# Optimization experiments

Hardware: AMD Instinct MI355X
Metric: run time of the kernel (lower is better)

The kernel has to match this reference:

```python
import jax, jax.numpy as jnp
import numpy as np

BATCH, T, D_MODEL, DIM = 8, 4096, 512, 512
R_MIN, R_MAX, MAX_PHASE = 0.0, 1.0, 6.28


def setup_inputs() -> dict:
    key = jax.random.key(0)
    ks = jax.random.split(key, 8)
    x = jax.random.normal(ks[0], (BATCH, T, D_MODEL), dtype=jnp.float32)
    h0 = jnp.zeros((BATCH, 1, DIM), dtype=jnp.float32)
    # nu_log / theta_log per the module's initializers
    u1 = jax.random.uniform(ks[1], (DIM,))
    nu_log = jnp.log(-0.5 * jnp.log(u1 * (R_MAX ** 2 - R_MIN ** 2) + R_MIN ** 2)).astype(jnp.float32)
    u2 = jax.random.uniform(ks[2], (DIM,))
    theta_log = jnp.log(MAX_PHASE * u2).astype(jnp.float32)
    # B ~ N(0,1)/sqrt(2*D_in), C ~ N(0,1)/sqrt(D_out)
    B_re = (jax.random.normal(ks[3], (D_MODEL, DIM)) / jnp.sqrt(2.0 * D_MODEL)).astype(jnp.float32)
    B_im = (jax.random.normal(ks[4], (D_MODEL, DIM)) / jnp.sqrt(2.0 * D_MODEL)).astype(jnp.float32)
    C_re = (jax.random.normal(ks[5], (DIM, D_MODEL)) / jnp.sqrt(float(D_MODEL))).astype(jnp.float32)
    C_im = (jax.random.normal(ks[6], (DIM, D_MODEL)) / jnp.sqrt(float(D_MODEL))).astype(jnp.float32)
    D_param = jax.random.normal(ks[7], (D_MODEL,)).astype(jnp.float32)
    # gamma_log = log(sqrt(1 - |Lambda|^2)) with Lambda from nu/theta
    diag_lambda = jnp.exp(-jnp.exp(nu_log) + 1j * jnp.exp(theta_log))
    gamma_log = jnp.log(jnp.sqrt(1.0 - jnp.abs(diag_lambda) ** 2)).astype(jnp.float32)
    return {"x": x, "h0": h0, "nu_log": nu_log, "theta_log": theta_log,
            "B_re": B_re, "B_im": B_im, "C_re": C_re, "C_im": C_im,
            "D_param": D_param, "gamma_log": gamma_log}


def _binary_op(ei, ej):
    a_i, b_i = ei
    a_j, b_j = ej
    return (a_j * a_i, a_j * b_i + b_j)


def reference(x, h0, nu_log, theta_log, B_re, B_im, C_re, C_im, D_param, gamma_log):
    B, T_len, _ = x.shape
    Lambda = jnp.exp(-jnp.exp(nu_log) + 1j * jnp.exp(theta_log))            # (N,) complex
    B_norm = (B_re + 1j * B_im) * jnp.exp(gamma_log)[None, :]               # (D,N) complex
    C = C_re + 1j * C_im                                                     # (N,D) complex
    # Input projection: Bu[b,t,n] = sum_d x[b,t,d] * B_norm[d,n]
    Bu = jnp.einsum('btd,dn->btn', x.astype(jnp.complex64), B_norm)
    Bu = jnp.concatenate([h0.astype(jnp.complex64), Bu], axis=1)             # (B,T+1,N)
    Lam = jnp.broadcast_to(Lambda, Bu.shape)                                 # (B,T+1,N)
    _, H = jax.lax.associative_scan(_binary_op, (Lam, Bu), axis=1)
    H = H[:, 1:]                                                             # (B,T,N)
    y = jnp.einsum('btn,nd->btd', H, C).real + D_param * x                   # (B,T,D)
    new_h = H[:, -1:]                                                        # (B,1,N) complex
    return (y, new_h)
```

## Files before the change

kernel.cpp:

```cpp
#include <hip/hip_runtime.h>

#define T_LEN 4096
#define DMODEL 512
#define DIM 512
#define NBATCH 8
#define MROWS (NBATCH * T_LEN)
#define NCHUNK 128
#define LCHUNK 32

typedef __attribute__((ext_vector_type(8))) short short8;
typedef __attribute__((ext_vector_type(4))) float float4v;

__device__ __forceinline__ ushort f2b(float f) {
    union { float fl; unsigned u; } v; v.fl = f;
    unsigned u = v.u;
    return (ushort)((u + 0x7FFFu + ((u >> 16) & 1u)) >> 16);
}
__device__ __forceinline__ float b2f(ushort u) {
    union { unsigned u; float f; } v; v.u = (unsigned)u << 16; return v.f;
}

__device__ __forceinline__ void glds16(const ushort* g, ushort* l) {
    __builtin_amdgcn_global_load_lds(
        (const __attribute__((address_space(1))) void*)g,
        (__attribute__((address_space(3))) void*)l, 16, 0, 0);
}


__global__ __launch_bounds__(256) void k_prep_x(const float* __restrict__ x,
                                                ushort* __restrict__ xb) {
    int i = (blockIdx.x * 256 + threadIdx.x) * 4;
    float4 v = *(const float4*)(x + i);
    ushort4 o;
    o.x = f2b(v.x); o.y = f2b(v.y); o.z = f2b(v.z); o.w = f2b(v.w);
    *(ushort4*)(xb + i) = o;
}

__global__ __launch_bounds__(256) void k_prep_B(const float* __restrict__ Bre,
                                                const float* __restrict__ Bim,
                                                const float* __restrict__ gamma_log,
                                                ushort* __restrict__ BT) {
    int idx = blockIdx.x * 256 + threadIdx.x;
    int n = idx >> 9;
    int d = idx & 511;
    float v;
    if (n < 512) v = Bre[d * 512 + n] * __expf(gamma_log[n]);
    else { int nn = n - 512; v = Bim[d * 512 + nn] * __expf(gamma_log[nn]); }
    BT[idx] = f2b(v);
}

__global__ __launch_bounds__(256) void k_prep_C(const float* __restrict__ Cre,
                                                const float* __restrict__ Cim,
                                                ushort* __restrict__ CT) {
    int idx = blockIdx.x * 256 + threadIdx.x;
    int d = idx >> 10;
    int k = idx & 1023;
    float v = (k < 512) ? Cre[k * 512 + d] : -Cim[(k - 512) * 512 + d];
    CT[idx] = f2b(v);
}

template<int K, int MODE, int NBN>
__global__ __launch_bounds__(256) void k_gemm(
    const ushort* __restrict__ A, const ushort* __restrict__ Bt,
    ushort* __restrict__ oRe, ushort* __restrict__ oIm,
    float* __restrict__ y, const float* __restrict__ x, const float* __restrict__ Dp) {
    __shared__ ushort sA[128 * 64];
    __shared__ ushort sB[128 * 64];
    const int tid = threadIdx.x;
    const int L = blockIdx.x;
    const int xcd = L & 7;
    const int slot = L >> 3;
    const int m0 = (xcd * 32 + slot / NBN) * 128;
    const int n0 = (slot % NBN) * 128;
    const int wave = tid >> 6;
    const int lane = tid & 63;
    const int wm = (wave >> 1) * 64;
    const int wn = (wave & 1) * 64;
    const int lr = lane & 15;
    const int quad = lane >> 4;

    const int srow = lane >> 3;
    const int schunk = (lane & 7) ^ srow;
    const ushort* gA0 = A + (size_t)(m0 + wave * 32 + srow) * K + schunk * 8;
    const ushort* gB0 = Bt + (size_t)(n0 + wave * 32 + srow) * K + schunk * 8;

    float4v acc[4][4];
#pragma unroll
    for (int i = 0; i < 4; i++)
#pragma unroll
        for (int j = 0; j < 4; j++) {
            float4v z = {0.f, 0.f, 0.f, 0.f};
            acc[i][j] = z;
        }

    for (int k0 = 0; k0 < K; k0 += 64) {
        __syncthreads();
#pragma unroll
        for (int c = 0; c < 4; c++) {
            glds16(gA0 + (size_t)(c * 8) * K + k0, &sA[(wave * 32 + c * 8) * 64]);
            glds16(gB0 + (size_t)(c * 8) * K + k0, &sB[(wave * 32 + c * 8) * 64]);
        }
        __syncthreads();

#pragma unroll
        for (int kk = 0; kk < 2; kk++) {
            short8 af[4], bfr[4];
#pragma unroll
            for (int i = 0; i < 4; i++) {
                int row = wm + i * 16 + lr;
                af[i] = *(const short8*)&sA[row * 64 + (((kk * 4 + quad) ^ (row & 7)) * 8)];
            }
#pragma unroll
            for (int j = 0; j < 4; j++) {
                int row = wn + j * 16 + lr;
                bfr[j] = *(const short8*)&sB[row * 64 + (((kk * 4 + quad) ^ (row & 7)) * 8)];
            }
#pragma unroll
            for (int i = 0; i < 4; i++)
#pragma unroll
                for (int j = 0; j < 4; j++)
                    acc[i][j] = __builtin_amdgcn_mfma_f32_16x16x32_bf16(af[i], bfr[j], acc[i][j], 0, 0, 0);
        }
    }

#pragma unroll
    for (int i = 0; i < 4; i++) {
#pragma unroll
        for (int j = 0; j < 4; j++) {
            int gmb = m0 + wm + i * 16 + quad * 4;
            int gn = n0 + wn + j * 16 + lr;
#pragma unroll
            for (int r = 0; r < 4; r++) {
                float v = acc[i][j][r];
                int row = gmb + r;
                if (MODE == 1) {
                    if (gn < 512) oRe[(size_t)row * 512 + gn] = f2b(v);
                    else oIm[(size_t)row * 512 + (gn - 512)] = f2b(v);
                } else {
                    size_t o = (size_t)row * 512 + gn;
                    y[o] = v + Dp[gn] * x[o];
                }
            }
        }
    }
}


__device__ __forceinline__ void lambda_of(const float* nu_log, const float* theta_log,
                                          int n, float& lre, float& lim) {
    float e = __expf(nu_log[n]);
    float th = __expf(theta_log[n]);
    float rad = __expf(-e);
    float s, c;
    __sincosf(th, &s, &c);
    lre = rad * c;
    lim = rad * s;
}

__global__ __launch_bounds__(256) void k_scan1(const ushort* __restrict__ BuRe,
                                               const ushort* __restrict__ BuIm,
                                               const float* __restrict__ nu_log,
                                               const float* __restrict__ theta_log,
                                               float* __restrict__ cRe, float* __restrict__ cIm) {
    int n2 = threadIdx.x;
    int b = blockIdx.x >> 7;
    int c = blockIdx.x & 127;
    float lre0, lim0, lre1, lim1;
    lambda_of(nu_log, theta_log, 2 * n2, lre0, lim0);
    lambda_of(nu_log, theta_log, 2 * n2 + 1, lre1, lim1);
    float hr0 = 0.f, hi0 = 0.f, hr1 = 0.f, hi1 = 0.f;
    size_t base = ((size_t)b * T_LEN + (size_t)c * LCHUNK) * 512 + 2 * n2;
#pragma unroll 8
    for (int j = 0; j < LCHUNK; j++) {
        ushort2 ur = *(const ushort2*)(BuRe + base + (size_t)j * 512);
        ushort2 ui = *(const ushort2*)(BuIm + base + (size_t)j * 512);
        float br0 = b2f(ur.x), br1 = b2f(ur.y), bi0 = b2f(ui.x), bi1 = b2f(ui.y);
        float nr0 = lre0 * hr0 - lim0 * hi0 + br0;
        float ni0 = lre0 * hi0 + lim0 * hr0 + bi0;
        hr0 = nr0; hi0 = ni0;
        float nr1 = lre1 * hr1 - lim1 * hi1 + br1;
        float ni1 = lre1 * hi1 + lim1 * hr1 + bi1;
        hr1 = nr1; hi1 = ni1;
    }
    size_t co = ((size_t)b * NCHUNK + c) * 512 + 2 * n2;
    *(float2*)(cRe + co) = make_float2(hr0, hr1);
    *(float2*)(cIm + co) = make_float2(hi0, hi1);
}

__global__ __launch_bounds__(64) void k_scan2(const float* __restrict__ cRe,
                                              const float* __restrict__ cIm,
                                              const float* __restrict__ h0,
                                              const float* __restrict__ nu_log,
                                              const float* __restrict__ theta_log,
                                              float* __restrict__ pRe, float* __restrict__ pIm,
                                              float* __restrict__ newH, int newh_mode) {
    int idx = blockIdx.x * 64 + threadIdx.x;
    int b = idx >> 9;
    int n = idx & 511;
    float lre, lim;
    lambda_of(nu_log, theta_log, n, lre, lim);
    float Lr = lre, Li = lim;
#pragma unroll
    for (int s = 0; s < 5; s++) {
        float nr = Lr * Lr - Li * Li;
        float ni = 2.f * Lr * Li;
        Lr = nr; Li = ni;
    }
    float cr = h0[b * 512 + n];
    float ci = 0.f;
#pragma unroll 4
    for (int c = 0; c < NCHUNK; c++) {
        size_t o = ((size_t)b * NCHUNK + c) * 512 + n;
        pRe[o] = cr;
        pIm[o] = ci;
        float ar = cRe[o], ai = cIm[o];
        float nr = Lr * cr - Li * ci + ar;
        float ni = Lr * ci + Li * cr + ai;
        cr = nr; ci = ni;
    }
    size_t ci_idx = (size_t)b * 512 + n;
    if (newh_mode == 1) {
        newH[ci_idx] = cr;
        newH[(size_t)NBATCH * 512 + ci_idx] = ci;
    } else if (newh_mode == 2) {
        newH[ci_idx] = cr;
    } else {
        newH[ci_idx * 2] = cr;
        newH[ci_idx * 2 + 1] = ci;
    }
}

__global__ __launch_bounds__(256) void k_scan3(const ushort* __restrict__ BuRe,
                                               const ushort* __restrict__ BuIm,
                                               const float* __restrict__ pRe,
                                               const float* __restrict__ pIm,
                                               const float* __restrict__ nu_log,
                                               const float* __restrict__ theta_log,
                                               ushort* __restrict__ Hbf) {
    int n2 = threadIdx.x;
    int b = blockIdx.x >> 7;
    int c = blockIdx.x & 127;
    float lre0, lim0, lre1, lim1;
    lambda_of(nu_log, theta_log, 2 * n2, lre0, lim0);
    lambda_of(nu_log, theta_log, 2 * n2 + 1, lre1, lim1);
    size_t co = ((size_t)b * NCHUNK + c) * 512 + 2 * n2;
    float2 frv = *(const float2*)(pRe + co);
    float2 fiv = *(const float2*)(pIm + co);
    float fr0 = frv.x, fr1 = frv.y, fi0 = fiv.x, fi1 = fiv.y;
    float pr0 = lre0, pi0 = lim0, pr1 = lre1, pi1 = lim1;
    float hr0 = 0.f, hi0 = 0.f, hr1 = 0.f, hi1 = 0.f;
    size_t row0 = (size_t)b * T_LEN + (size_t)c * LCHUNK;
#pragma unroll 4
    for (int j = 0; j < LCHUNK; j++) {
        size_t base = (row0 + j) * 512 + 2 * n2;
        ushort2 ur = *(const ushort2*)(BuRe + base);
        ushort2 ui = *(const ushort2*)(BuIm + base);
        float br0 = b2f(ur.x), br1 = b2f(ur.y), bi0 = b2f(ui.x), bi1 = b2f(ui.y);
        float nr0 = lre0 * hr0 - lim0 * hi0 + br0;
        float ni0 = lre0 * hi0 + lim0 * hr0 + bi0;
        hr0 = nr0; hi0 = ni0;
        float nr1 = lre1 * hr1 - lim1 * hi1 + br1;
        float ni1 = lre1 * hi1 + lim1 * hr1 + bi1;
        hr1 = nr1; hi1 = ni1;
        float vr0 = hr0 + pr0 * fr0 - pi0 * fi0;
        float vi0 = hi0 + pr0 * fi0 + pi0 * fr0;
        float vr1 = hr1 + pr1 * fr1 - pi1 * fi1;
        float vi1 = hi1 + pr1 * fi1 + pi1 * fr1;
        size_t hrow = (row0 + j) * 1024;
        ushort2 wre, wim;
        wre.x = f2b(vr0); wre.y = f2b(vr1);
        wim.x = f2b(vi0); wim.y = f2b(vi1);
        *(ushort2*)(Hbf + hrow + 2 * n2) = wre;
        *(ushort2*)(Hbf + hrow + 512 + 2 * n2) = wim;
        float npr0 = pr0 * lre0 - pi0 * lim0;
        float npi0 = pr0 * lim0 + pi0 * lre0;
        pr0 = npr0; pi0 = npi0;
        float npr1 = pr1 * lre1 - pi1 * lim1;
        float npi1 = pr1 * lim1 + pi1 * lre1;
        pr1 = npr1; pi1 = npi1;
    }
}


extern "C" void kernel_launch(void* const* d_in, const int* in_sizes, int n_in,
                              void* d_out, int out_size, void* d_ws, size_t ws_size,
                              hipStream_t stream) {
    const float* x         = (const float*)d_in[0];
    const float* h0        = (const float*)d_in[1];
    const float* nu_log    = (const float*)d_in[2];
    const float* theta_log = (const float*)d_in[3];
    const float* B_re      = (const float*)d_in[4];
    const float* B_im      = (const float*)d_in[5];
    const float* C_re      = (const float*)d_in[6];
    const float* C_im      = (const float*)d_in[7];
    const float* D_param   = (const float*)d_in[8];
    const float* gamma_log = (const float*)d_in[9];

    char* ws = (char*)d_ws;
    size_t off = 0;
    ushort* Xb   = (ushort*)(ws + off); off += (size_t)MROWS * 512 * 2;
    ushort* BT   = (ushort*)(ws + off); off += (size_t)1024 * 512 * 2;
    ushort* CT   = (ushort*)(ws + off); off += (size_t)512 * 1024 * 2;
    ushort* BuRe = (ushort*)(ws + off); off += (size_t)MROWS * 512 * 2;
    ushort* BuIm = (ushort*)(ws + off); off += (size_t)MROWS * 512 * 2;
    ushort* Hbf  = (ushort*)(ws + off); off += (size_t)MROWS * 1024 * 2;
    float*  cRe  = (float*)(ws + off); off += (size_t)NBATCH * NCHUNK * 512 * 4;
    float*  cIm  = (float*)(ws + off); off += (size_t)NBATCH * NCHUNK * 512 * 4;
    float*  pRe  = (float*)(ws + off); off += (size_t)NBATCH * NCHUNK * 512 * 4;
    float*  pIm  = (float*)(ws + off); off += (size_t)NBATCH * NCHUNK * 512 * 4;

    float* y_out = (float*)d_out;
    float* newH  = (float*)d_out + (size_t)MROWS * 512;

    const int tail = out_size - MROWS * 512;
    int newh_mode = 0;
    if (tail == NBATCH * 512 * 2) newh_mode = 1;
    else if (tail == NBATCH * 512) newh_mode = 2;

    k_prep_x<<<dim3(MROWS * 512 / 4 / 256), dim3(256), 0, stream>>>(x, Xb);
    k_prep_B<<<dim3(1024 * 512 / 256), dim3(256), 0, stream>>>(B_re, B_im, gamma_log, BT);
    k_prep_C<<<dim3(512 * 1024 / 256), dim3(256), 0, stream>>>(C_re, C_im, CT);

    k_gemm<512, 1, 8><<<dim3(2048), dim3(256), 0, stream>>>(
        Xb, BT, BuRe, BuIm, nullptr, nullptr, nullptr);

    k_scan1<<<dim3(NBATCH * NCHUNK), dim3(256), 0, stream>>>(BuRe, BuIm, nu_log, theta_log, cRe, cIm);
    k_scan2<<<dim3(NBATCH * 512 / 64), dim3(64), 0, stream>>>(cRe, cIm, h0, nu_log, theta_log, pRe, pIm, newH, newh_mode);
    k_scan3<<<dim3(NBATCH * NCHUNK), dim3(256), 0, stream>>>(BuRe, BuIm, pRe, pIm, nu_log, theta_log, Hbf);

    k_gemm<1024, 2, 4><<<dim3(1024), dim3(256), 0, stream>>>(
        Hbf, CT, nullptr, nullptr, y_out, x, D_param);
}
```

Baseline: 292.5 us.

## Store Bu channel-major, vectorize scan loads, merge prep kernels, halve chunk count

The first GEMM now writes Bu transposed (channel-major, time contiguous) as 4-wide bf16 stores. This lets scan1 and scan3 read 8 consecutive timesteps per channel with 16-byte loads instead of strided 4-byte loads. The chunk split changes from 128x32 to 64x64, and the chunk-power exponent in scan2 is adjusted to match. The three prep kernels are merged into one launch. The risks are per-thread strided access across channels in the scan (each thread touches different rows) and fewer blocks in the scan kernels.

New measurement: 421.5 us. 44.1% more time.

```diff
diff --git a/kernel.cpp b/kernel.cpp
--- a/kernel.cpp
+++ b/kernel.cpp
@@ -5,8 +5,8 @@
 #define DIM 512
 #define NBATCH 8
 #define MROWS (NBATCH * T_LEN)
-#define NCHUNK 128
-#define LCHUNK 32
+#define NCHUNK 64
+#define LCHUNK 64
 
 typedef __attribute__((ext_vector_type(8))) short short8;
 typedef __attribute__((ext_vector_type(4))) float float4v;
@@ -19,6 +19,12 @@
 __device__ __forceinline__ float b2f(ushort u) {
     union { unsigned u; float f; } v; v.u = (unsigned)u << 16; return v.f;
 }
+__device__ __forceinline__ float bflo(unsigned u) {
+    union { unsigned x; float f; } v; v.x = u << 16; return v.f;
+}
+__device__ __forceinline__ float bfhi(unsigned u) {
+    union { unsigned x; float f; } v; v.x = u & 0xffff0000u; return v.f;
+}
 
 __device__ __forceinline__ void glds16(const ushort* g, ushort* l) {
     __builtin_amdgcn_global_load_lds(
@@ -26,37 +32,38 @@
         (__attribute__((address_space(3))) void*)l, 16, 0, 0);
 }
 
-
-__global__ __launch_bounds__(256) void k_prep_x(const float* __restrict__ x,
-                                                ushort* __restrict__ xb) {
-    int i = (blockIdx.x * 256 + threadIdx.x) * 4;
-    float4 v = *(const float4*)(x + i);
-    ushort4 o;
-    o.x = f2b(v.x); o.y = f2b(v.y); o.z = f2b(v.z); o.w = f2b(v.w);
-    *(ushort4*)(xb + i) = o;
-}
-
-__global__ __launch_bounds__(256) void k_prep_B(const float* __restrict__ Bre,
-                                                const float* __restrict__ Bim,
-                                                const float* __restrict__ gamma_log,
-                                                ushort* __restrict__ BT) {
-    int idx = blockIdx.x * 256 + threadIdx.x;
-    int n = idx >> 9;
-    int d = idx & 511;
-    float v;
-    if (n < 512) v = Bre[d * 512 + n] * __expf(gamma_log[n]);
-    else { int nn = n - 512; v = Bim[d * 512 + nn] * __expf(gamma_log[nn]); }
-    BT[idx] = f2b(v);
-}
-
-__global__ __launch_bounds__(256) void k_prep_C(const float* __restrict__ Cre,
-                                                const float* __restrict__ Cim,
-                                                ushort* __restrict__ CT) {
-    int idx = blockIdx.x * 256 + threadIdx.x;
-    int d = idx >> 10;
-    int k = idx & 1023;
-    float v = (k < 512) ? Cre[k * 512 + d] : -Cim[(k - 512) * 512 + d];
-    CT[idx] = f2b(v);
+#define NBX (MROWS * 512 / 4 / 256)
+__global__ __launch_bounds__(256) void k_prep(const float* __restrict__ x,
+                                              const float* __restrict__ Bre,
+                                              const float* __restrict__ Bim,
+                                              const float* __restrict__ gamma_log,
+                                              const float* __restrict__ Cre,
+                                              const float* __restrict__ Cim,
+                                              ushort* __restrict__ xb,
+                                              ushort* __restrict__ BT,
+                                              ushort* __restrict__ CT) {
+    int blk = blockIdx.x;
+    if (blk < NBX) {
+        int i = (blk * 256 + threadIdx.x) * 4;
+        float4 v = *(const float4*)(x + i);
+        ushort4 o;
+        o.x = f2b(v.x); o.y = f2b(v.y); o.z = f2b(v.z); o.w = f2b(v.w);
+        *(ushort4*)(xb + i) = o;
+    } else if (blk < NBX + 2048) {
+        int idx = (blk - NBX) * 256 + threadIdx.x;
+        int n = idx >> 9;
+        int d = idx & 511;
+        float v;
+        if (n < 512) v = Bre[d * 512 + n] * __expf(gamma_log[n]);
+        else { int nn = n - 512; v = Bim[d * 512 + nn] * __expf(gamma_log[nn]); }
+        BT[idx] = f2b(v);
+    } else {
+        int idx = (blk - NBX - 2048) * 256 + threadIdx.x;
+        int d = idx >> 10;
+        int k = idx & 1023;
+        float v = (k < 512) ? Cre[k * 512 + d] : -Cim[(k - 512) * 512 + d];
+        CT[idx] = f2b(v);
+    }
 }
 
 template<int K, int MODE, int NBN>
@@ -127,18 +134,20 @@
     for (int i = 0; i < 4; i++) {
 #pragma unroll
         for (int j = 0; j < 4; j++) {
-            int gmb = m0 + wm + i * 16 + quad * 4;
+            int m = m0 + wm + i * 16 + quad * 4;
             int gn = n0 + wn + j * 16 + lr;
-#pragma unroll
-            for (int r = 0; r < 4; r++) {
-                float v = acc[i][j][r];
-                int row = gmb + r;
-                if (MODE == 1) {
-                    if (gn < 512) oRe[(size_t)row * 512 + gn] = f2b(v);
-                    else oIm[(size_t)row * 512 + (gn - 512)] = f2b(v);
-                } else {
-                    size_t o = (size_t)row * 512 + gn;
-                    y[o] = v + Dp[gn] * x[o];
+            if (MODE == 1) {
+                ushort4 h;
+                h.x = f2b(acc[i][j][0]); h.y = f2b(acc[i][j][1]);
+                h.z = f2b(acc[i][j][2]); h.w = f2b(acc[i][j][3]);
+                ushort* dst = (gn < 512) ? (oRe + (size_t)gn * MROWS + m)
+                                         : (oIm + (size_t)(gn - 512) * MROWS + m);
+                *(ushort4*)dst = h;
+            } else {
+#pragma unroll
+                for (int r = 0; r < 4; r++) {
+                    size_t o = (size_t)(m + r) * 512 + gn;
+                    y[o] = acc[i][j][r] + Dp[gn] * x[o];
                 }
             }
         }
@@ -163,24 +172,43 @@
                                                const float* __restrict__ theta_log,
                                                float* __restrict__ cRe, float* __restrict__ cIm) {
     int n2 = threadIdx.x;
-    int b = blockIdx.x >> 7;
-    int c = blockIdx.x & 127;
+    int b = blockIdx.x >> 6;
+    int c = blockIdx.x & 63;
+    int ch0 = 2 * n2, ch1 = 2 * n2 + 1;
     float lre0, lim0, lre1, lim1;
-    lambda_of(nu_log, theta_log, 2 * n2, lre0, lim0);
-    lambda_of(nu_log, theta_log, 2 * n2 + 1, lre1, lim1);
+    lambda_of(nu_log, theta_log, ch0, lre0, lim0);
+    lambda_of(nu_log, theta_log, ch1, lre1, lim1);
+    size_t mb = (size_t)b * T_LEN + (size_t)c * LCHUNK;
+    const ushort* p0r = BuRe + (size_t)ch0 * MROWS + mb;
+    const ushort* p1r = BuRe + (size_t)ch1 * MROWS + mb;
+    const ushort* p0i = BuIm + (size_t)ch0 * MROWS + mb;
+    const ushort* p1i = BuIm + (size_t)ch1 * MROWS + mb;
     float hr0 = 0.f, hi0 = 0.f, hr1 = 0.f, hi1 = 0.f;
-    size_t base = ((size_t)b * T_LEN + (size_t)c * LCHUNK) * 512 + 2 * n2;
-#pragma unroll 8
-    for (int j = 0; j < LCHUNK; j++) {
-        ushort2 ur = *(const ushort2*)(BuRe + base + (size_t)j * 512);
-        ushort2 ui = *(const ushort2*)(BuIm + base + (size_t)j * 512);
-        float br0 = b2f(ur.x), br1 = b2f(ur.y), bi0 = b2f(ui.x), bi1 = b2f(ui.y);
-        float nr0 = lre0 * hr0 - lim0 * hi0 + br0;
-        float ni0 = lre0 * hi0 + lim0 * hr0 + bi0;
-        hr0 = nr0; hi0 = ni0;
-        float nr1 = lre1 * hr1 - lim1 * hi1 + br1;
-        float ni1 = lre1 * hi1 + lim1 * hr1 + bi1;
-        hr1 = nr1; hi1 = ni1;
+    for (int g = 0; g < LCHUNK / 8; g++) {
+        uint4 r0 = *(const uint4*)(p0r + g * 8);
+        uint4 i0 = *(const uint4*)(p0i + g * 8);
+        uint4 r1 = *(const uint4*)(p1r + g * 8);
+        uint4 i1 = *(const uint4*)(p1i + g * 8);
+        unsigned rw0[4] = {r0.x, r0.y, r0.z, r0.w};
+        unsigned iw0[4] = {i0.x, i0.y, i0.z, i0.w};
+        unsigned rw1[4] = {r1.x, r1.y, r1.z, r1.w};
+        unsigned iw1[4] = {i1.x, i1.y, i1.z, i1.w};
+#pragma unroll
+        for (int q = 0; q < 4; q++) {
+            float br, bi, nr, ni;
+            br = bflo(rw0[q]); bi = bflo(iw0[q]);
+            nr = lre0 * hr0 - lim0 * hi0 + br; ni = lre0 * hi0 + lim0 * hr0 + bi;
+            hr0 = nr; hi0 = ni;
+            br = bfhi(rw0[q]); bi = bfhi(iw0[q]);
+            nr = lre0 * hr0 - lim0 * hi0 + br; ni = lre0 * hi0 + lim0 * hr0 + bi;
+            hr0 = nr; hi0 = ni;
+            br = bflo(rw1[q]); bi = bflo(iw1[q]);
+            nr = lre1 * hr1 - lim1 * hi1 + br; ni = lre1 * hi1 + lim1 * hr1 + bi;
+            hr1 = nr; hi1 = ni;
+            br = bfhi(rw1[q]); bi = bfhi(iw1[q]);
+            nr = lre1 * hr1 - lim1 * hi1 + br; ni = lre1 * hi1 + lim1 * hr1 + bi;
+            hr1 = nr; hi1 = ni;
+        }
     }
     size_t co = ((size_t)b * NCHUNK + c) * 512 + 2 * n2;
     *(float2*)(cRe + co) = make_float2(hr0, hr1);
@@ -201,7 +229,7 @@
     lambda_of(nu_log, theta_log, n, lre, lim);
     float Lr = lre, Li = lim;
 #pragma unroll
-    for (int s = 0; s < 5; s++) {
+    for (int s = 0; s < 6; s++) {
         float nr = Lr * Lr - Li * Li;
         float ni = 2.f * Lr * Li;
         Lr = nr; Li = ni;
@@ -238,46 +266,65 @@
                                                const float* __restrict__ theta_log,
                                                ushort* __restrict__ Hbf) {
     int n2 = threadIdx.x;
-    int b = blockIdx.x >> 7;
-    int c = blockIdx.x & 127;
+    int b = blockIdx.x >> 6;
+    int c = blockIdx.x & 63;
+    int ch0 = 2 * n2, ch1 = 2 * n2 + 1;
     float lre0, lim0, lre1, lim1;
-    lambda_of(nu_log, theta_log, 2 * n2, lre0, lim0);
-    lambda_of(nu_log, theta_log, 2 * n2 + 1, lre1, lim1);
+    lambda_of(nu_log, theta_log, ch0, lre0, lim0);
+    lambda_of(nu_log, theta_log, ch1, lre1, lim1);
     size_t co = ((size_t)b * NCHUNK + c) * 512 + 2 * n2;
     float2 frv = *(const float2*)(pRe + co);
     float2 fiv = *(const float2*)(pIm + co);
     float fr0 = frv.x, fr1 = frv.y, fi0 = fiv.x, fi1 = fiv.y;
     float pr0 = lre0, pi0 = lim0, pr1 = lre1, pi1 = lim1;
     float hr0 = 0.f, hi0 = 0.f, hr1 = 0.f, hi1 = 0.f;
-    size_t row0 = (size_t)b * T_LEN + (size_t)c * LCHUNK;
-#pragma unroll 4
-    for (int j = 0; j < LCHUNK; j++) {
-        size_t base = (row0 + j) * 512 + 2 * n2;
-        ushort2 ur = *(const ushort2*)(BuRe + base);
-        ushort2 ui = *(const ushort2*)(BuIm + base);
-        float br0 = b2f(ur.x), br1 = b2f(ur.y), bi0 = b2f(ui.x), bi1 = b2f(ui.y);
-        float nr0 = lre0 * hr0 - lim0 * hi0 + br0;
-        float ni0 = lre0 * hi0 + lim0 * hr0 + bi0;
-        hr0 = nr0; hi0 = ni0;
-        float nr1 = lre1 * hr1 - lim1 * hi1 + br1;
-        float ni1 = lre1 * hi1 + lim1 * hr1 + bi1;
-        hr1 = nr1; hi1 = ni1;
-        float vr0 = hr0 + pr0 * fr0 - pi0 * fi0;
-        float vi0 = hi0 + pr0 * fi0 + pi0 * fr0;
-        float vr1 = hr1 + pr1 * fr1 - pi1 * fi1;
-        float vi1 = hi1 + pr1 * fi1 + pi1 * fr1;
-        size_t hrow = (row0 + j) * 1024;
-        ushort2 wre, wim;
-        wre.x = f2b(vr0); wre.y = f2b(vr1);
-        wim.x = f2b(vi0); wim.y = f2b(vi1);
-        *(ushort2*)(Hbf + hrow + 2 * n2) = wre;
-        *(ushort2*)(Hbf + hrow + 512 + 2 * n2) = wim;
-        float npr0 = pr0 * lre0 - pi0 * lim0;
-        float npi0 = pr0 * lim0 + pi0 * lre0;
-        pr0 = npr0; pi0 = npi0;
-        float npr1 = pr1 * lre1 - pi1 * lim1;
-        float npi1 = pr1 * lim1 + pi1 * lre1;
-        pr1 = npr1; pi1 = npi1;
+    size_t mb = (size_t)b * T_LEN + (size_t)c * LCHUNK;
+    const ushort* p0r = BuRe + (size_t)ch0 * MROWS + mb;
+    const ushort* p1r = BuRe + (size_t)ch1 * MROWS + mb;
+    const ushort* p0i = BuIm + (size_t)ch0 * MROWS + mb;
+    const ushort* p1i = BuIm + (size_t)ch1 * MROWS + mb;
+    for (int g = 0; g < LCHUNK / 8; g++) {
+        uint4 r0 = *(const uint4*)(p0r + g * 8);
+        uint4 i0 = *(const uint4*)(p0i + g * 8);
+        uint4 r1 = *(const uint4*)(p1r + g * 8);
+        uint4 i1 = *(const uint4*)(p1i + g * 8);
+        unsigned rw0[4] = {r0.x, r0.y, r0.z, r0.w};
+        unsigned iw0[4] = {i0.x, i0.y, i0.z, i0.w};
+        unsigned rw1[4] = {r1.x, r1.y, r1.z, r1.w};
+        unsigned iw1[4] = {i1.x, i1.y, i1.z, i1.w};
+#pragma unroll
+        for (int q = 0; q < 4; q++) {
+#pragma unroll
+            for (int hlf = 0; hlf < 2; hlf++) {
+                float br0 = hlf ? bfhi(rw0[q]) : bflo(rw0[q]);
+                float bi0 = hlf ? bfhi(iw0[q]) : bflo(iw0[q]);
+                float br1 = hlf ? bfhi(rw1[q]) : bflo(rw1[q]);
+                float bi1 = hlf ? bfhi(iw1[q]) : bflo(iw1[q]);
+                float nr0 = lre0 * hr0 - lim0 * hi0 + br0;
+                float ni0 = lre0 * hi0 + lim0 * hr0 + bi0;
+                hr0 = nr0; hi0 = ni0;
+                float nr1 = lre1 * hr1 - lim1 * hi1 + br1;
+                float ni1 = lre1 * hi1 + lim1 * hr1 + bi1;
+                hr1 = nr1; hi1 = ni1;
+                float vr0 = hr0 + pr0 * fr0 - pi0 * fi0;
+                float vi0 = hi0 + pr0 * fi0 + pi0 * fr0;
+                float vr1 = hr1 + pr1 * fr1 - pi1 * fi1;
+                float vi1 = hi1 + pr1 * fi1 + pi1 * fr1;
+                int j = g * 8 + q * 2 + hlf;
+                size_t hrow = (mb + j) * 1024;
+                ushort2 wre, wim;
+                wre.x = f2b(vr0); wre.y = f2b(vr1);
+                wim.x = f2b(vi0); wim.y = f2b(vi1);
+                *(ushort2*)(Hbf + hrow + 2 * n2) = wre;
+                *(ushort2*)(Hbf + hrow + 512 + 2 * n2) = wim;
+                float npr0 = pr0 * lre0 - pi0 * lim0;
+                float npi0 = pr0 * lim0 + pi0 * lre0;
+                pr0 = npr0; pi0 = npi0;
+                float npr1 = pr1 * lre1 - pi1 * lim1;
+                float npi1 = pr1 * lim1 + pi1 * lre1;
+                pr1 = npr1; pi1 = npi1;
+            }
+        }
     }
 }
 
@@ -317,9 +364,8 @@
     if (tail == NBATCH * 512 * 2) newh_mode = 1;
     else if (tail == NBATCH * 512) newh_mode = 2;
 
-    k_prep_x<<<dim3(MROWS * 512 / 4 / 256), dim3(256), 0, stream>>>(x, Xb);
-    k_prep_B<<<dim3(1024 * 512 / 256), dim3(256), 0, stream>>>(B_re, B_im, gamma_log, BT);
-    k_prep_C<<<dim3(512 * 1024 / 256), dim3(256), 0, stream>>>(C_re, C_im, CT);
+    k_prep<<<dim3(NBX + 4096), dim3(256), 0, stream>>>(x, B_re, B_im, gamma_log, C_re, C_im,
+                                                       Xb, BT, CT);
 
     k_gemm<512, 1, 8><<<dim3(2048), dim3(256), 0, stream>>>(
         Xb, BT, BuRe, BuIm, nullptr, nullptr, nullptr);
```
